# Optimization experiments

Measured on AMD Instinct MI355X. Metric: run time of the kernel, lower is better.

The kernel has to match this reference:

```python
import jax, jax.numpy as jnp
import numpy as np

N_NODES = 50000
N_EDGES = 800000
DIM = 128
LAYERS = 3


def setup_inputs() -> dict:
    key = jax.random.key(0)
    k1, k2, k3, k4 = jax.random.split(key, 4)
    x = jax.random.normal(k1, (N_NODES, DIM), dtype=jnp.float32)
    edge_index = jax.random.randint(k2, (2, N_EDGES), 0, N_NODES, dtype=jnp.int64)
    scale = 1.0 / np.sqrt(DIM)
    W_rel = jax.random.normal(k3, (LAYERS, DIM, DIM), dtype=jnp.float32) * scale
    W_root = jax.random.normal(k4, (LAYERS, DIM, DIM), dtype=jnp.float32) * scale
    b = jnp.zeros((LAYERS, DIM), dtype=jnp.float32)
    return {"x": x, "edge_index": edge_index, "W_rel": W_rel, "W_root": W_root, "b": b}


def graph_conv(x, src, dst, w_rel, w_root, bias):
    # message: gather source node features along each edge  [E, D]
    msg = x[src]
    # add-aggregation per destination node                  [N, D]
    agg = jax.ops.segment_sum(msg, dst, num_segments=N_NODES)
    # out_i = W_rel @ agg_i + W_root @ x_i + b
    return agg @ w_rel + x @ w_root + bias


def reference(x, edge_index, W_rel, W_root, b):
    src, dst = edge_index[0], edge_index[1]
    for l in range(LAYERS):
        x = graph_conv(x, src, dst, W_rel[l], W_root[l], b[l])
    return x
```

## Files before the change

kernel.cpp:

```cpp
#include <hip/hip_runtime.h>

#define N_NODES 50000
#define N_EDGES 800000
#define DIM     128
#define LAYERS  3

#define BSHIFT    7
#define N_BUCKETS 391
#define CHUNK     16384
#define N_CHUNKS  49

using short8 = __attribute__((ext_vector_type(8))) short;
using f32x4  = __attribute__((ext_vector_type(4))) float;

__device__ __forceinline__ unsigned short f2bf(float f) {
    unsigned int u = __builtin_bit_cast(unsigned int, f);
    unsigned int r = (u + 0x7fffu + ((u >> 16) & 1u)) >> 16;
    return (unsigned short)r;
}
__device__ __forceinline__ float bfl(unsigned int u) {
    return __builtin_bit_cast(float, u << 16);
}
__device__ __forceinline__ float bfh(unsigned int u) {
    return __builtin_bit_cast(float, u & 0xffff0000u);
}


__global__ __launch_bounds__(256) void convert_x(const float* __restrict__ x,
                                                 unsigned short* __restrict__ xb) {
    int t = blockIdx.x * 256 + threadIdx.x;
    size_t base = (size_t)t * 8;
    if (base >= (size_t)N_NODES * DIM) return;
    float4 v0 = *(const float4*)(x + base);
    float4 v1 = *(const float4*)(x + base + 4);
    uint4 o;
    o.x = ((unsigned)f2bf(v0.y) << 16) | f2bf(v0.x);
    o.y = ((unsigned)f2bf(v0.w) << 16) | f2bf(v0.z);
    o.z = ((unsigned)f2bf(v1.y) << 16) | f2bf(v1.x);
    o.w = ((unsigned)f2bf(v1.w) << 16) | f2bf(v1.z);
    *(uint4*)(xb + base) = o;
}

__global__ __launch_bounds__(256) void prep_w(const float* __restrict__ Wrel,
                                              const float* __restrict__ Wroot,
                                              unsigned short* __restrict__ Wt) {
    int t = blockIdx.x * 256 + threadIdx.x;
    if (t >= LAYERS * 2 * 128 * 32) return;
    int k4  = t & 31;
    int col = (t >> 5) & 127;
    int mat = (t >> 12) & 1;
    int l   = t >> 13;
    const float* W = (mat ? Wroot : Wrel) + (size_t)l * DIM * DIM;
    int k0 = k4 * 4;
    unsigned short b0 = f2bf(W[(size_t)(k0 + 0) * DIM + col]);
    unsigned short b1 = f2bf(W[(size_t)(k0 + 1) * DIM + col]);
    unsigned short b2 = f2bf(W[(size_t)(k0 + 2) * DIM + col]);
    unsigned short b3 = f2bf(W[(size_t)(k0 + 3) * DIM + col]);
    uint2 o;
    o.x = ((unsigned)b1 << 16) | b0;
    o.y = ((unsigned)b3 << 16) | b2;
    *(uint2*)(Wt + (size_t)l * 128 * 256 + (size_t)col * 256 + mat * 128 + k0) = o;
}


__global__ __launch_bounds__(1024) void bin_count(const int* __restrict__ dst,
                                                  int* __restrict__ bcnt) {
    __shared__ int hist[N_BUCKETS];
    int tid = threadIdx.x, chunk = blockIdx.x;
    for (int t = tid; t < N_BUCKETS; t += 1024) hist[t] = 0;
    __syncthreads();
    int base = chunk * CHUNK;
    for (int i = 0; i < CHUNK; i += 1024) {
        int e = base + i + tid;
        if (e < N_EDGES) atomicAdd(&hist[dst[e] >> BSHIFT], 1);
    }
    __syncthreads();
    for (int t = tid; t < N_BUCKETS; t += 1024)
        bcnt[t * N_CHUNKS + chunk] = hist[t];
}

__global__ __launch_bounds__(64) void bscan_a(const int* __restrict__ bcnt,
                                              int* __restrict__ boff,
                                              int* __restrict__ btot) {
    __shared__ int sh[64];
    int b = blockIdx.x, j = threadIdx.x;
    int v = (j < N_CHUNKS) ? bcnt[b * N_CHUNKS + j] : 0;
    sh[j] = v;
    __syncthreads();
    for (int off = 1; off < 64; off <<= 1) {
        int t = (j >= off) ? sh[j - off] : 0;
        __syncthreads();
        sh[j] += t;
        __syncthreads();
    }
    if (j < N_CHUNKS) boff[b * N_CHUNKS + j] = sh[j] - v;
    if (j == 63) btot[b] = sh[63];
}

__global__ __launch_bounds__(512) void bscan_b(const int* __restrict__ btot,
                                               int* __restrict__ bucket_start) {
    __shared__ int sh[512];
    int j = threadIdx.x;
    int v = (j < N_BUCKETS) ? btot[j] : 0;
    sh[j] = v;
    __syncthreads();
    for (int off = 1; off < 512; off <<= 1) {
        int t = (j >= off) ? sh[j - off] : 0;
        __syncthreads();
        sh[j] += t;
        __syncthreads();
    }
    if (j < N_BUCKETS) bucket_start[j] = sh[j] - v;
    if (j == N_BUCKETS - 1) bucket_start[N_BUCKETS] = sh[j];
}

__global__ __launch_bounds__(1024) void bin_scatter(const int* __restrict__ src,
                                                    const int* __restrict__ dst,
                                                    const int* __restrict__ bucket_start,
                                                    const int* __restrict__ boff,
                                                    unsigned int* __restrict__ pairs) {
    __shared__ int cur[N_BUCKETS];
    int tid = threadIdx.x, chunk = blockIdx.x;
    for (int t = tid; t < N_BUCKETS; t += 1024)
        cur[t] = bucket_start[t] + boff[t * N_CHUNKS + chunk];
    __syncthreads();
    int base = chunk * CHUNK;
    for (int i = 0; i < CHUNK; i += 1024) {
        int e = base + i + tid;
        if (e < N_EDGES) {
            int d = dst[e];
            int b = d >> BSHIFT;
            int p = atomicAdd(&cur[b], 1);
            pairs[p] = ((unsigned)(d & 127) << 16) | (unsigned)src[e];
        }
    }
}

__global__ __launch_bounds__(1024) void fill_lds(const unsigned int* __restrict__ pairs,
                                                 const int* __restrict__ bucket_start,
                                                 int* __restrict__ row_start,
                                                 unsigned short* __restrict__ srcs16) {
    __shared__ int hist[128];
    __shared__ int offs[128];
    __shared__ int cur[128];
    __shared__ unsigned short srt[4096];
    int b = blockIdx.x, tid = threadIdx.x;
    int s0 = bucket_start[b], s1 = bucket_start[b + 1];
    int cnt = s1 - s0;
    if (tid < 128) hist[tid] = 0;
    __syncthreads();
    for (int k = tid; k < cnt; k += 1024)
        atomicAdd(&hist[pairs[s0 + k] >> 16], 1);
    __syncthreads();
    if (tid < 128) offs[tid] = hist[tid];
    __syncthreads();
    for (int off = 1; off < 128; off <<= 1) {
        int t = 0;
        if (tid < 128 && tid >= off) t = offs[tid - off];
        __syncthreads();
        if (tid < 128) offs[tid] += t;
        __syncthreads();
    }
    if (tid < 128) {
        int excl = offs[tid] - hist[tid];
        cur[tid] = excl;
        int node = b * 128 + tid;
        if (node <= N_NODES) row_start[node] = s0 + excl;
    }
    __syncthreads();
    for (int k = tid; k < cnt; k += 1024) {
        unsigned int u = pairs[s0 + k];
        int p = atomicAdd(&cur[u >> 16], 1);
        srt[p] = (unsigned short)(u & 0xffffu);
    }
    __syncthreads();
    for (int k = tid; k < cnt; k += 1024)
        srcs16[s0 + k] = srt[k];
}


__device__ __forceinline__ void acc8(float* a, uint4 v) {
    a[0] += bfl(v.x); a[1] += bfh(v.x);
    a[2] += bfl(v.y); a[3] += bfh(v.y);
    a[4] += bfl(v.z); a[5] += bfh(v.z);
    a[6] += bfl(v.w); a[7] += bfh(v.w);
}

__global__ __launch_bounds__(256) void aggregate_bf16(const unsigned short* __restrict__ xb,
                                                      const int* __restrict__ row_start,
                                                      const unsigned short* __restrict__ srcs,
                                                      unsigned short* __restrict__ aggb) {
    int tid  = threadIdx.x;
    int L    = tid & 15;
    int node = blockIdx.x * 16 + (tid >> 4);
    if (node >= N_NODES) return;
    int beg = row_start[node];
    int end = row_start[node + 1];

    const uint4* xq = (const uint4*)xb;
    float a[8] = {0.f, 0.f, 0.f, 0.f, 0.f, 0.f, 0.f, 0.f};

    int j = beg;
    for (; j + 3 < end; j += 4) {
        uint4 v0 = xq[(size_t)srcs[j]     * 16 + L];
        uint4 v1 = xq[(size_t)srcs[j + 1] * 16 + L];
        uint4 v2 = xq[(size_t)srcs[j + 2] * 16 + L];
        uint4 v3 = xq[(size_t)srcs[j + 3] * 16 + L];
        acc8(a, v0); acc8(a, v1); acc8(a, v2); acc8(a, v3);
    }
    for (; j < end; ++j) {
        uint4 v = xq[(size_t)srcs[j] * 16 + L];
        acc8(a, v);
    }

    uint4 o;
    o.x = ((unsigned)f2bf(a[1]) << 16) | f2bf(a[0]);
    o.y = ((unsigned)f2bf(a[3]) << 16) | f2bf(a[2]);
    o.z = ((unsigned)f2bf(a[5]) << 16) | f2bf(a[4]);
    o.w = ((unsigned)f2bf(a[7]) << 16) | f2bf(a[6]);
    ((uint4*)aggb)[(size_t)node * 16 + L] = o;
}


#define LDP 72

__global__ __launch_bounds__(256) void gemm_bf16(const unsigned short* __restrict__ aggb,
                                                 const unsigned short* __restrict__ xb,
                                                 const unsigned short* __restrict__ Wt_l,
                                                 const float* __restrict__ bias,
                                                 unsigned short* __restrict__ outb,
                                                 float* __restrict__ outf) {
    __shared__ unsigned short As[128 * LDP];
    __shared__ unsigned short Bs[128 * LDP];

    int tid = threadIdx.x;
    int lane = tid & 63;
    int wave = tid >> 6;
    int wm = wave >> 1;
    int wn = wave & 1;
    int row0 = blockIdx.x * 128;

    f32x4 acc[4][4];
#pragma unroll
    for (int m = 0; m < 4; ++m)
#pragma unroll
        for (int n = 0; n < 4; ++n) acc[m][n] = (f32x4){0.f, 0.f, 0.f, 0.f};

    for (int s = 0; s < 4; ++s) {
        const unsigned short* Asrc = (s < 2) ? aggb : xb;
        int k0 = (s & 1) * 64;

#pragma unroll
        for (int i = 0; i < 4; ++i) {
            int c = tid + i * 256;
            int r = c >> 3, sg = c & 7;
            int gr = row0 + r;
            uint4 v = {0u, 0u, 0u, 0u};
            if (gr < N_NODES) v = *(const uint4*)(Asrc + (size_t)gr * DIM + k0 + sg * 8);
            *(uint4*)&As[r * LDP + sg * 8] = v;
        }
#pragma unroll
        for (int i = 0; i < 4; ++i) {
            int c = tid + i * 256;
            int col = c >> 3, sg = c & 7;
            *(uint4*)&Bs[col * LDP + sg * 8] =
                *(const uint4*)(Wt_l + (size_t)col * 256 + s * 64 + sg * 8);
        }
        __syncthreads();

#pragma unroll
        for (int kk = 0; kk < 64; kk += 32) {
            short8 a[4], b[4];
#pragma unroll
            for (int m = 0; m < 4; ++m)
                a[m] = *(const short8*)&As[(wm * 64 + m * 16 + (lane & 15)) * LDP + kk + (lane >> 4) * 8];
#pragma unroll
            for (int n = 0; n < 4; ++n)
                b[n] = *(const short8*)&Bs[(wn * 64 + n * 16 + (lane & 15)) * LDP + kk + (lane >> 4) * 8];
#pragma unroll
            for (int m = 0; m < 4; ++m)
#pragma unroll
                for (int n = 0; n < 4; ++n)
                    acc[m][n] = __builtin_amdgcn_mfma_f32_16x16x32_bf16(a[m], b[n], acc[m][n], 0, 0, 0);
        }
        __syncthreads();
    }

#pragma unroll
    for (int n = 0; n < 4; ++n) {
        int col = wn * 64 + n * 16 + (lane & 15);
        float bv = bias[col];
#pragma unroll
        for (int m = 0; m < 4; ++m) {
            int rbase = row0 + wm * 64 + m * 16 + (lane >> 4) * 4;
#pragma unroll
            for (int r = 0; r < 4; ++r) {
                int row = rbase + r;
                if (row < N_NODES) {
                    float v = acc[m][n][r] + bv;
                    if (outf) outf[(size_t)row * DIM + col] = v;
                    else      outb[(size_t)row * DIM + col] = f2bf(v);
                }
            }
        }
    }
}


extern "C" void kernel_launch(void* const* d_in, const int* in_sizes, int n_in,
                              void* d_out, int out_size, void* d_ws, size_t ws_size,
                              hipStream_t stream) {
    const float* x0    = (const float*)d_in[0];
    const int*   ei    = (const int*)d_in[1];
    const float* Wrel  = (const float*)d_in[2];
    const float* Wroot = (const float*)d_in[3];
    const float* bvec  = (const float*)d_in[4];
    float* out = (float*)d_out;

    char* ws = (char*)d_ws;
    const size_t XB = (size_t)N_NODES * DIM * sizeof(unsigned short);
    unsigned short* xbA  = (unsigned short*)ws;
    unsigned short* xbB  = (unsigned short*)(ws + XB);
    unsigned short* aggb = (unsigned short*)(ws + 2 * XB);
    unsigned int* pairs  = (unsigned int*)(ws + 2 * XB);
    int* bcnt            = (int*)(ws + 2 * XB + 3200000);
    int* boff            = (int*)(ws + 2 * XB + 3276800);
    int* btot            = (int*)(ws + 2 * XB + 3353600);
    int* bucket_start    = (int*)(ws + 2 * XB + 3355648);
    unsigned short* Wt   = (unsigned short*)(ws + 3 * XB);
    unsigned short* srcs16 = (unsigned short*)(ws + 3 * XB + 196608);
    int* row_start       = (int*)(ws + 3 * XB + 196608 + 1600000);

    const int* src = ei;
    const int* dst = ei + N_EDGES;

    convert_x<<<(N_NODES * DIM / 8 + 255) / 256, 256, 0, stream>>>(x0, xbA);
    prep_w<<<(LAYERS * 2 * 128 * 32 + 255) / 256, 256, 0, stream>>>(Wrel, Wroot, Wt);

    bin_count<<<N_CHUNKS, 1024, 0, stream>>>(dst, bcnt);
    bscan_a<<<N_BUCKETS, 64, 0, stream>>>(bcnt, boff, btot);
    bscan_b<<<1, 512, 0, stream>>>(btot, bucket_start);
    bin_scatter<<<N_CHUNKS, 1024, 0, stream>>>(src, dst, bucket_start, boff, pairs);
    fill_lds<<<N_BUCKETS, 1024, 0, stream>>>(pairs, bucket_start, row_start, srcs16);

    unsigned short* xin = xbA;
    unsigned short* xouts[LAYERS] = {xbB, xbA, nullptr};
    for (int l = 0; l < LAYERS; ++l) {
        aggregate_bf16<<<(N_NODES + 15) / 16, 256, 0, stream>>>(xin, row_start, srcs16, aggb);
        gemm_bf16<<<(N_NODES + 127) / 128, 256, 0, stream>>>(
            aggb, xin, Wt + (size_t)l * 128 * 256, bvec + (size_t)l * DIM,
            xouts[l], (l == LAYERS - 1) ? out : nullptr);
        xin = xouts[l];
    }
}
```

Measured before the change: 260.1 us.

## Keep full weight tile in swizzled LDS and load A fragments directly from global

The GEMM kernel now loads the whole 128x256 transposed weight matrix into LDS once, using an XOR swizzle to avoid bank conflicts. The per-stage A staging through shared memory and the barriers between stages are removed. Each wave now owns 32 rows and all 128 output columns and reads its A fragments straight from global memory. This cuts LDS traffic and synchronisation, but uses 64KB of LDS per block, which may limit occupancy, and the direct global A reads are less coalesced.

```diff
diff --git a/kernel.cpp b/kernel.cpp
--- a/kernel.cpp
+++ b/kernel.cpp
@@ -222,80 +222,70 @@
 }
 
 
-#define LDP 72
-
 __global__ __launch_bounds__(256) void gemm_bf16(const unsigned short* __restrict__ aggb,
                                                  const unsigned short* __restrict__ xb,
                                                  const unsigned short* __restrict__ Wt_l,
                                                  const float* __restrict__ bias,
                                                  unsigned short* __restrict__ outb,
                                                  float* __restrict__ outf) {
-    __shared__ unsigned short As[128 * LDP];
-    __shared__ unsigned short Bs[128 * LDP];
-
-    int tid = threadIdx.x;
+    __shared__ unsigned short Bs[128 * 256];
+
+    int tid  = threadIdx.x;
     int lane = tid & 63;
-    int wave = tid >> 6;
-    int wm = wave >> 1;
-    int wn = wave & 1;
-    int row0 = blockIdx.x * 128;
-
-    f32x4 acc[4][4];
-#pragma unroll
-    for (int m = 0; m < 4; ++m)
-#pragma unroll
-        for (int n = 0; n < 4; ++n) acc[m][n] = (f32x4){0.f, 0.f, 0.f, 0.f};
-
-    for (int s = 0; s < 4; ++s) {
-        const unsigned short* Asrc = (s < 2) ? aggb : xb;
-        int k0 = (s & 1) * 64;
-
-#pragma unroll
-        for (int i = 0; i < 4; ++i) {
-            int c = tid + i * 256;
-            int r = c >> 3, sg = c & 7;
-            int gr = row0 + r;
-            uint4 v = {0u, 0u, 0u, 0u};
-            if (gr < N_NODES) v = *(const uint4*)(Asrc + (size_t)gr * DIM + k0 + sg * 8);
-            *(uint4*)&As[r * LDP + sg * 8] = v;
+    int w    = tid >> 6;
+
+#pragma unroll
+    for (int i = 0; i < 16; ++i) {
+        int c   = tid + i * 256;
+        int col = c >> 5;
+        int q   = c & 31;
+        uint4 v = ((const uint4*)Wt_l)[c];
+        *(uint4*)&Bs[col * 256 + 8 * (q ^ (col & 7))] = v;
+    }
+    __syncthreads();
+
+    int row0 = blockIdx.x * 128 + w * 32;
+
+    f32x4 acc[2][8];
+#pragma unroll
+    for (int m = 0; m < 2; ++m)
+#pragma unroll
+        for (int n = 0; n < 8; ++n) acc[m][n] = (f32x4){0.f, 0.f, 0.f, 0.f};
+
+    const short8 zero8 = {0, 0, 0, 0, 0, 0, 0, 0};
+
+#pragma unroll
+    for (int ch = 0; ch < 8; ++ch) {
+        const unsigned short* Asrc = (ch < 4) ? aggb : xb;
+        int k0 = (ch & 3) * 32 + (lane >> 4) * 8;
+
+        short8 a[2];
+#pragma unroll
+        for (int m = 0; m < 2; ++m) {
+            int r = row0 + m * 16 + (lane & 15);
+            a[m] = (r < N_NODES) ? *(const short8*)(Asrc + (size_t)r * DIM + k0) : zero8;
         }
-#pragma unroll
-        for (int i = 0; i < 4; ++i) {
-            int c = tid + i * 256;
-            int col = c >> 3, sg = c & 7;
-            *(uint4*)&Bs[col * LDP + sg * 8] =
-                *(const uint4*)(Wt_l + (size_t)col * 256 + s * 64 + sg * 8);
+
+        int qbase = ch * 4 + (lane >> 4);
+#pragma unroll
+        for (int n = 0; n < 8; ++n) {
+            int col = n * 16 + (lane & 15);
+            short8 b = *(const short8*)&Bs[col * 256 + 8 * (qbase ^ (col & 7))];
+            acc[0][n] = __builtin_amdgcn_mfma_f32_16x16x32_bf16(a[0], b, acc[0][n], 0, 0, 0);
+            acc[1][n] = __builtin_amdgcn_mfma_f32_16x16x32_bf16(a[1], b, acc[1][n], 0, 0, 0);
         }
-        __syncthreads();
-
-#pragma unroll
-        for (int kk = 0; kk < 64; kk += 32) {
-            short8 a[4], b[4];
-#pragma unroll
-            for (int m = 0; m < 4; ++m)
-                a[m] = *(const short8*)&As[(wm * 64 + m * 16 + (lane & 15)) * LDP + kk + (lane >> 4) * 8];
-#pragma unroll
-            for (int n = 0; n < 4; ++n)
-                b[n] = *(const short8*)&Bs[(wn * 64 + n * 16 + (lane & 15)) * LDP + kk + (lane >> 4) * 8];
-#pragma unroll
-            for (int m = 0; m < 4; ++m)
-#pragma unroll
-                for (int n = 0; n < 4; ++n)
-                    acc[m][n] = __builtin_amdgcn_mfma_f32_16x16x32_bf16(a[m], b[n], acc[m][n], 0, 0, 0);
-        }
-        __syncthreads();
-    }
-
-#pragma unroll
-    for (int n = 0; n < 4; ++n) {
-        int col = wn * 64 + n * 16 + (lane & 15);
+    }
+
+#pragma unroll
+    for (int n = 0; n < 8; ++n) {
+        int col = n * 16 + (lane & 15);
         float bv = bias[col];
 #pragma unroll
-        for (int m = 0; m < 4; ++m) {
-            int rbase = row0 + wm * 64 + m * 16 + (lane >> 4) * 4;
+        for (int m = 0; m < 2; ++m) {
+            int rb = row0 + m * 16 + (lane >> 4) * 4;
 #pragma unroll
             for (int r = 0; r < 4; ++r) {
-                int row = rbase + r;
+                int row = rb + r;
                 if (row < N_NODES) {
                     float v = acc[m][n][r] + bv;
                     if (outf) outf[(size_t)row * DIM + col] = v;
```

New measurement: 255.7 us. No clear change (-1.7%).
